# Optimization experiments

Measured on AMD Instinct MI355X. Metric: run time of the kernel, lower is better.

Reference implementation:

```python
import jax, jax.numpy as jnp
import numpy as np

TEMP = 0.1
TEMP_SUP = 0.5
PROP = 0.5  # proportion_pure_contrastive
SIGMA = 1.0
GAMMA = 1.0 / (2.0 * SIGMA ** 2)
INF = 1e8


def _l2norm(x, eps=1e-12):
    # torch F.normalize: x / max(||x||, eps)
    n = jnp.sqrt(jnp.sum(x * x, axis=-1, keepdims=True))
    return x / jnp.maximum(n, eps)


def _cross_entropy(logits, targets):
    # mean over rows of -log_softmax(logits)[i, targets[i]]
    logp = jax.nn.log_softmax(logits, axis=-1)
    return -jnp.mean(jnp.take_along_axis(logp, targets[:, None], axis=-1))


def setup_inputs() -> dict:
    key = jax.random.key(0)
    k1, k2, k3 = jax.random.split(key, 3)
    N, D = 4096, 256
    z_i = jax.random.normal(k1, (N, D), dtype=jnp.float32)
    z_j = jax.random.normal(k2, (N, D), dtype=jnp.float32)
    labels = jax.random.normal(k3, (N, 1), dtype=jnp.float32)
    return {"z_i": z_i, "z_j": z_j, "labels": labels}


def _forward(z_i, z_j, labels):
    N = z_i.shape[0]
    eye = jnp.eye(N, dtype=z_i.dtype)
    zin = _l2norm(z_i)
    zjn = _l2norm(z_j)

    # ---- pure contrastive branch (temperature TEMP) ----
    sim_zii = zin @ zin.T / TEMP - INF * eye
    sim_zjj = zjn @ zjn.T / TEMP - INF * eye
    sim_zij = zin @ zjn.T / TEMP
    correct = jnp.arange(N, dtype=jnp.int32)
    loss_i = _cross_entropy(jnp.concatenate([sim_zij, sim_zii], axis=1), correct)
    loss_j = _cross_entropy(jnp.concatenate([sim_zij.T, sim_zjj], axis=1), correct)
    loss_pure = loss_i + loss_j

    # ---- supervised branch (temperature TEMP_SUP) ----
    s_zii = zin @ zin.T / TEMP_SUP - INF * eye
    s_zjj = zjn @ zjn.T / TEMP_SUP - INF * eye
    s_zij = zin @ zjn.T / TEMP_SUP

    # RBF kernel on duplicated labels (detached in original -> stop_gradient)
    all_lab = jnp.tile(labels.reshape(N, -1), (2, 1))  # [2N, L]
    all_lab = jax.lax.stop_gradient(all_lab)
    sq = jnp.sum(all_lab * all_lab, axis=1)
    d2 = sq[:, None] + sq[None, :] - 2.0 * (all_lab @ all_lab.T)
    weights = jnp.exp(-GAMMA * jnp.maximum(d2, 0.0))  # [2N, 2N]
    weights = weights * (1.0 - jnp.eye(2 * N, dtype=weights.dtype))
    norm = jnp.sum(weights, axis=1, keepdims=True)  # [2N, 1]
    weights = weights / norm
    weights_norm = weights * jnp.log(norm)

    sim_Z = jnp.concatenate([
        jnp.concatenate([s_zii, s_zij], axis=1),
        jnp.concatenate([s_zij.T, s_zjj], axis=1),
    ], axis=0)  # [2N, 2N]
    log_sim_Z = jax.nn.log_softmax(sim_Z, axis=1)
    loss_sup = (-1.0 / N) * jnp.sum(weights * log_sim_Z)
    loss_sup += (-1.0 / N) * jnp.sum(weights_norm)

    return PROP * loss_pure + (1.0 - PROP) * loss_sup


def reference(z_i, z_j, labels):
    return _forward(z_i, z_j, labels)
```

## Files before the change

kernel.cpp:

```cpp
#include <hip/hip_runtime.h>
#include <hip/hip_bf16.h>

#define NN 4096
#define DD 256

typedef __attribute__((ext_vector_type(8))) short bf16x8;
typedef __attribute__((ext_vector_type(4))) float f32x4;

#define LOG2E 1.44269504088896f

typedef const unsigned int __attribute__((address_space(1)))* gu32p;
typedef unsigned int __attribute__((address_space(3)))* su32p;

__device__ __forceinline__ float fexp2(float x) { return __builtin_amdgcn_exp2f(x); }

__global__ __launch_bounds__(256) void k_norm(const float* __restrict__ zi,
                                              const float* __restrict__ zj,
                                              __hip_bfloat16* __restrict__ oi,
                                              __hip_bfloat16* __restrict__ oj) {
  int gw = (blockIdx.x * 256 + threadIdx.x) >> 6;
  int lane = threadIdx.x & 63;
  const float* src = (gw < NN) ? zi : zj;
  __hip_bfloat16* dst = (gw < NN) ? oi : oj;
  int row = (gw < NN) ? gw : gw - NN;
  float4 v = ((const float4*)(src + (size_t)row * DD))[lane];
  float ss = v.x * v.x + v.y * v.y + v.z * v.z + v.w * v.w;
#pragma unroll
  for (int m = 1; m < 64; m <<= 1) ss += __shfl_xor(ss, m);
  float s = 1.0f / fmaxf(sqrtf(ss), 1e-12f);
  __hip_bfloat16* d = dst + (size_t)row * DD + lane * 4;
  d[0] = __float2bfloat16(v.x * s);
  d[1] = __float2bfloat16(v.y * s);
  d[2] = __float2bfloat16(v.z * s);
  d[3] = __float2bfloat16(v.w * s);
}

template <int MODE>
__device__ __forceinline__ void epi(
    const f32x4 acc[2][4], const float labr[2][4], const float* __restrict__ labels,
    float rA[2][4], float rB[2][4], float rC[2][4], float rT[2][4],
    float* __restrict__ diag, int rowbase, int colbase, int wave, int fr, int kg) {
#pragma unroll
  for (int cf = 0; cf < 4; ++cf) {
    const int cg = colbase + cf * 16 + fr;
    const float labc = labels[cg];
#pragma unroll
    for (int sub = 0; sub < 2; ++sub) {
#pragma unroll
      for (int reg = 0; reg < 4; ++reg) {
        float S = acc[sub][cf][reg];
        float b = fexp2(fmaf(2.f * LOG2E, S, -2.f * LOG2E));
        float b2 = b * b;
        float b5 = b2 * b2 * b;
        float dl = labr[sub][reg] - labc;
        float kk = fexp2(dl * dl * (-0.5f * LOG2E));
        float ks = kk * S;
        if (MODE != 0) {
          const int rg = rowbase + wave * 32 + sub * 16 + kg * 4 + reg;
          if (MODE == 1) {
            if (rg == cg) diag[rg] = S;
          }
          if (MODE == 2) {
            if (rg == cg) { b = 0.f; b5 = 0.f; ks = 0.f; kk = 0.f; }
          }
        }
        rA[sub][reg] += b5;
        rB[sub][reg] += b;
        rC[sub][reg] += ks;
        rT[sub][reg] += kk;
      }
    }
  }
}

__global__ __launch_bounds__(256, 2) void k_main(
    const __hip_bfloat16* __restrict__ zin, const __hip_bfloat16* __restrict__ zjn,
    const float* __restrict__ labels,
    float* __restrict__ part, float* __restrict__ diag) {
  __shared__ short lB[64 * 256];

  const int cc = blockIdx.x;
  const int by = blockIdx.y;
  const int combo = blockIdx.z;

  const __hip_bfloat16* Ap = (combo == 1 || combo == 3) ? zjn : zin;
  const __hip_bfloat16* Bp = (combo == 1 || combo == 2) ? zin : zjn;
  const int rS0 = (combo == 0) ? 0 : (combo == 1) ? 2 : (combo == 2) ? 1 : 3;
  const bool wantT = (combo == 2);

  const int tid = threadIdx.x;
  const int lane = tid & 63;
  const int wave = tid >> 6;
  const int fr = lane & 15;
  const int kg = lane >> 4;
  const int rowbase = by * 128;
  char* lBc = (char*)lB;

  bf16x8 a[2][8];
#pragma unroll
  for (int sub = 0; sub < 2; ++sub) {
    const __hip_bfloat16* Ar =
        Ap + (size_t)(rowbase + wave * 32 + sub * 16 + fr) * DD + kg * 8;
#pragma unroll
    for (int k = 0; k < 8; ++k) a[sub][k] = *(const bf16x8*)(Ar + k * 32);
  }

  float labr[2][4];
#pragma unroll
  for (int sub = 0; sub < 2; ++sub)
#pragma unroll
    for (int reg = 0; reg < 4; ++reg)
      labr[sub][reg] = labels[rowbase + wave * 32 + sub * 16 + kg * 4 + reg];

  float rA[2][4] = {}, rB[2][4] = {}, rC[2][4] = {}, rT[2][4] = {};

  const int frb = (fr >> 2) & 1;
  const int P0 = fr * 512 + ((kg ^ (fr & 3)) << 4) + (frb << 6);

  const int dt0 = by * 2 - cc * 16;

#define STAGE(t)                                                              \
  {                                                                           \
    const char* Bt = (const char*)Bp + (size_t)(cc * 1024 + (t) * 64) * 512;  \
    _Pragma("unroll") for (int j = 0; j < 8; ++j) {                           \
      int f = tid + 256 * j;                                                  \
      int g = f ^ ((f >> 5) & 7);                                             \
      __builtin_amdgcn_global_load_lds(                                       \
          (gu32p)(const void*)(Bt + (size_t)g * 16),                          \
          (su32p)(void*)(lBc + (wave * 64 + 256 * j) * 16), 16, 0, 0);        \
    }                                                                         \
  }

  STAGE(0);

  for (int t = 0; t < 16; ++t) {
    __syncthreads();

    f32x4 acc[2][4];
#pragma unroll
    for (int s2 = 0; s2 < 2; ++s2)
#pragma unroll
      for (int cf = 0; cf < 4; ++cf) acc[s2][cf] = (f32x4){0.f, 0.f, 0.f, 0.f};

#pragma unroll
    for (int k = 0; k < 8; ++k) {
      const char* bbase = lBc + (P0 ^ (k << 6));
#pragma unroll
      for (int cf = 0; cf < 4; ++cf) {
        bf16x8 bv = *(const bf16x8*)(bbase + cf * 8192);
        acc[0][cf] = __builtin_amdgcn_mfma_f32_16x16x32_bf16(a[0][k], bv, acc[0][cf], 0, 0, 0);
        acc[1][cf] = __builtin_amdgcn_mfma_f32_16x16x32_bf16(a[1][k], bv, acc[1][cf], 0, 0, 0);
      }
    }

    __syncthreads();
    if (t < 15) STAGE(t + 1);

    const int colbase = cc * 1024 + t * 64;
    if (combo != 1 && (unsigned)(t - dt0) < 2u) {
      if (combo == 0)
        epi<1>(acc, labr, labels, rA, rB, rC, rT, diag, rowbase, colbase, wave, fr, kg);
      else
        epi<2>(acc, labr, labels, rA, rB, rC, rT, diag, rowbase, colbase, wave, fr, kg);
    } else {
      epi<0>(acc, labr, labels, rA, rB, rC, rT, diag, rowbase, colbase, wave, fr, kg);
    }
  }

  float* pc = part + (size_t)cc * 13 * NN;
#pragma unroll
  for (int sub = 0; sub < 2; ++sub)
#pragma unroll
    for (int reg = 0; reg < 4; ++reg) {
      float va = rA[sub][reg], vb = rB[sub][reg];
      float vc = rC[sub][reg], vt = rT[sub][reg];
#pragma unroll
      for (int m = 1; m < 16; m <<= 1) {
        va += __shfl_xor(va, m);
        vb += __shfl_xor(vb, m);
        vc += __shfl_xor(vc, m);
        vt += __shfl_xor(vt, m);
      }
      if (fr == 0) {
        int rg = rowbase + wave * 32 + sub * 16 + kg * 4 + reg;
        pc[rS0 * NN + rg] = va;
        pc[(rS0 + 4) * NN + rg] = vb;
        pc[(rS0 + 8) * NN + rg] = vc;
        if (wantT) pc[12 * NN + rg] = vt;
      }
    }
}

__global__ __launch_bounds__(256) void k_final(const float* __restrict__ part,
                                               const float* __restrict__ diag,
                                               float* __restrict__ out) {
  int i = blockIdx.x * 256 + threadIdx.x;
  float st[13];
#pragma unroll
  for (int p = 0; p < 13; ++p) {
    float s = 0.f;
#pragma unroll
    for (int c = 0; c < 4; ++c) s += part[((size_t)c * 13 + p) * NN + i];
    st[p] = s;
  }
  float d = diag[i];
  float accP = logf(st[0] + st[1]) + logf(st[2] + st[3]) + 20.f - 20.f * d;
  float nrm = 2.f * st[12] + 1.f;
  float W = 2.f * (st[8] + st[9] + st[10] + st[11]) / nrm;
  float lse = logf(st[4] + st[5]) + logf(st[6] + st[7]) + 4.f;
  float accS = lse - W - 2.f * logf(nrm);
  float v = accP + accS;
#pragma unroll
  for (int m = 1; m < 64; m <<= 1) v += __shfl_xor(v, m);
  __shared__ float red[4];
  if ((threadIdx.x & 63) == 0) red[threadIdx.x >> 6] = v;
  __syncthreads();
  if (threadIdx.x == 0) {
    float s = red[0] + red[1] + red[2] + red[3];
    atomicAdd(out, 0.5f * s / (float)NN);
  }
}

extern "C" void kernel_launch(void* const* d_in, const int* in_sizes, int n_in,
                              void* d_out, int out_size, void* d_ws, size_t ws_size,
                              hipStream_t stream) {
  const float* zi = (const float*)d_in[0];
  const float* zj = (const float*)d_in[1];
  const float* labels = (const float*)d_in[2];
  float* out = (float*)d_out;

  char* ws = (char*)d_ws;
  __hip_bfloat16* zinH = (__hip_bfloat16*)ws;
  __hip_bfloat16* zjnH = (__hip_bfloat16*)(ws + (size_t)NN * DD * 2);
  float* part = (float*)(ws + (size_t)NN * DD * 4);
  float* diag = part + 4 * 13 * NN;

  hipMemsetAsync(out, 0, sizeof(float), stream);

  k_norm<<<2 * NN / 4, 256, 0, stream>>>(zi, zj, zinH, zjnH);

  dim3 grid(4, NN / 128, 4);
  k_main<<<grid, 256, 0, stream>>>(zinH, zjnH, labels, part, diag);

  k_final<<<NN / 256, 256, 0, stream>>>(part, diag, out);
}
```

Before: 77.08 us.

## Exploit zi·zj transpose symmetry to drop fourth GEMM combo via column sums

Removes the separate zj·ziᵀ GEMM by computing column-wise partial sums (exp terms and kernel-weighted sims) of the zi·zjᵀ tile in the same pass, reducing work from four Gram blocks to three. It also splits columns across eight chunks instead of four, raises the occupancy hint to three blocks per CU, and packs the epilogue math into two-wide float vectors. The cost is extra shuffle reductions, shared-memory column buffers and a larger partial-sum buffer that the final kernel must read back. The label-kernel normalisation now comes from combo 0 rows, with the diagonal handled by a -1 correction.

```diff
diff --git a/kernel.cpp b/kernel.cpp
--- a/kernel.cpp
+++ b/kernel.cpp
@@ -3,11 +3,13 @@
 
 #define NN 4096
 #define DD 256
+#define CCN 8
+#define TPB 8
+#define LOG2E 1.44269504088896f
 
 typedef __attribute__((ext_vector_type(8))) short bf16x8;
 typedef __attribute__((ext_vector_type(4))) float f32x4;
-
-#define LOG2E 1.44269504088896f
+typedef __attribute__((ext_vector_type(2))) float f32x2;
 
 typedef const unsigned int __attribute__((address_space(1)))* gu32p;
 typedef unsigned int __attribute__((address_space(3)))* su32p;
@@ -35,58 +37,72 @@
   d[3] = __float2bfloat16(v.w * s);
 }
 
-template <int MODE>
+template <int MODE, bool COL>
 __device__ __forceinline__ void epi(
-    const f32x4 acc[2][4], const float labr[2][4], const float* __restrict__ labels,
-    float rA[2][4], float rB[2][4], float rC[2][4], float rT[2][4],
-    float* __restrict__ diag, int rowbase, int colbase, int wave, int fr, int kg) {
+    const f32x4 acc[2][4], const f32x2 labr[2][2], const float* __restrict__ labels,
+    f32x2 rA[2][2], f32x2 rB[2][2], f32x2 rC[2][2], f32x2 rT[2][2],
+    float cw[4][3], float* __restrict__ diag,
+    int rowbase, int colbase, int wave, int fr, int kg) {
 #pragma unroll
   for (int cf = 0; cf < 4; ++cf) {
     const int cg = colbase + cf * 16 + fr;
     const float labc = labels[cg];
+    const f32x2 labc2 = {labc, labc};
 #pragma unroll
     for (int sub = 0; sub < 2; ++sub) {
 #pragma unroll
-      for (int reg = 0; reg < 4; ++reg) {
-        float S = acc[sub][cf][reg];
-        float b = fexp2(fmaf(2.f * LOG2E, S, -2.f * LOG2E));
-        float b2 = b * b;
-        float b5 = b2 * b2 * b;
-        float dl = labr[sub][reg] - labc;
-        float kk = fexp2(dl * dl * (-0.5f * LOG2E));
-        float ks = kk * S;
+      for (int pp = 0; pp < 2; ++pp) {
+        f32x2 S = {acc[sub][cf][2 * pp], acc[sub][cf][2 * pp + 1]};
+        f32x2 arg = S * (2.f * LOG2E) + (-2.f * LOG2E);
+        f32x2 b;
+        b.x = fexp2(arg.x);
+        b.y = fexp2(arg.y);
+        f32x2 b2 = b * b;
+        f32x2 b5 = b2 * b2 * b;
+        f32x2 dl = labr[sub][pp] - labc2;
+        f32x2 e = (dl * (-0.5f * LOG2E)) * dl;
+        f32x2 kk;
+        kk.x = fexp2(e.x);
+        kk.y = fexp2(e.y);
+        f32x2 ks = kk * S;
         if (MODE != 0) {
-          const int rg = rowbase + wave * 32 + sub * 16 + kg * 4 + reg;
+          const int rg = rowbase + wave * 32 + sub * 16 + kg * 4 + 2 * pp;
           if (MODE == 1) {
-            if (rg == cg) diag[rg] = S;
+            if (rg == cg) diag[cg] = S.x;
+            if (rg + 1 == cg) diag[cg] = S.y;
+          } else {
+            if (rg == cg)     { b5.x = 0.f; b.x = 0.f; ks.x = 0.f; }
+            if (rg + 1 == cg) { b5.y = 0.f; b.y = 0.f; ks.y = 0.f; }
           }
-          if (MODE == 2) {
-            if (rg == cg) { b = 0.f; b5 = 0.f; ks = 0.f; kk = 0.f; }
-          }
-        }
-        rA[sub][reg] += b5;
-        rB[sub][reg] += b;
-        rC[sub][reg] += ks;
-        rT[sub][reg] += kk;
+        }
+        rA[sub][pp] += b5;
+        rB[sub][pp] += b;
+        rC[sub][pp] += ks;
+        if (COL) {
+          rT[sub][pp] += kk;
+          cw[cf][0] += b5.x + b5.y;
+          cw[cf][1] += b.x + b.y;
+          cw[cf][2] += ks.x + ks.y;
+        }
       }
     }
   }
 }
 
-__global__ __launch_bounds__(256, 2) void k_main(
+__global__ __launch_bounds__(256, 3) void k_main(
     const __hip_bfloat16* __restrict__ zin, const __hip_bfloat16* __restrict__ zjn,
     const float* __restrict__ labels,
-    float* __restrict__ part, float* __restrict__ diag) {
+    float* __restrict__ part, float* __restrict__ colp, float* __restrict__ diag) {
   __shared__ short lB[64 * 256];
+  __shared__ float colw[4][3][64];
 
   const int cc = blockIdx.x;
   const int by = blockIdx.y;
   const int combo = blockIdx.z;
-
-  const __hip_bfloat16* Ap = (combo == 1 || combo == 3) ? zjn : zin;
-  const __hip_bfloat16* Bp = (combo == 1 || combo == 2) ? zin : zjn;
-  const int rS0 = (combo == 0) ? 0 : (combo == 1) ? 2 : (combo == 2) ? 1 : 3;
-  const bool wantT = (combo == 2);
+  const bool COLF = (combo == 0);
+
+  const __hip_bfloat16* Ap = (combo == 2) ? zjn : zin;
+  const __hip_bfloat16* Bp = (combo == 1) ? zin : zjn;
 
   const int tid = threadIdx.x;
   const int lane = tid & 63;
@@ -105,36 +121,44 @@
     for (int k = 0; k < 8; ++k) a[sub][k] = *(const bf16x8*)(Ar + k * 32);
   }
 
-  float labr[2][4];
+  f32x2 labr[2][2];
 #pragma unroll
   for (int sub = 0; sub < 2; ++sub)
 #pragma unroll
-    for (int reg = 0; reg < 4; ++reg)
-      labr[sub][reg] = labels[rowbase + wave * 32 + sub * 16 + kg * 4 + reg];
-
-  float rA[2][4] = {}, rB[2][4] = {}, rC[2][4] = {}, rT[2][4] = {};
+    for (int pp = 0; pp < 2; ++pp) {
+      const float* lp = labels + rowbase + wave * 32 + sub * 16 + kg * 4 + 2 * pp;
+      labr[sub][pp] = (f32x2){lp[0], lp[1]};
+    }
+
+  f32x2 rA[2][2] = {}, rB[2][2] = {}, rC[2][2] = {}, rT[2][2] = {};
 
   const int frb = (fr >> 2) & 1;
   const int P0 = fr * 512 + ((kg ^ (fr & 3)) << 4) + (frb << 6);
 
-  const int dt0 = by * 2 - cc * 16;
-
-#define STAGE(t)                                                              \
-  {                                                                           \
-    const char* Bt = (const char*)Bp + (size_t)(cc * 1024 + (t) * 64) * 512;  \
-    _Pragma("unroll") for (int j = 0; j < 8; ++j) {                           \
-      int f = tid + 256 * j;                                                  \
-      int g = f ^ ((f >> 5) & 7);                                             \
-      __builtin_amdgcn_global_load_lds(                                       \
-          (gu32p)(const void*)(Bt + (size_t)g * 16),                          \
-          (su32p)(void*)(lBc + (wave * 64 + 256 * j) * 16), 16, 0, 0);        \
-    }                                                                         \
-  }
-
-  STAGE(0);
-
-  for (int t = 0; t < 16; ++t) {
+  auto stage = [&](int t) {
+    const char* Bt = (const char*)Bp + (size_t)(cc * 512 + t * 64) * 512;
+#pragma unroll
+    for (int j = 0; j < 8; ++j) {
+      int f = tid + 256 * j;
+      int g = f ^ ((f >> 5) & 7);
+      __builtin_amdgcn_global_load_lds(
+          (gu32p)(const void*)(Bt + (size_t)g * 16),
+          (su32p)(void*)(lBc + (wave * 64 + 256 * j) * 16), 16, 0, 0);
+    }
+  };
+  auto flushcol = [&](int t) {
+    if (tid < 192) {
+      int p = tid >> 6, c = tid & 63;
+      float v = colw[0][p][c] + colw[1][p][c] + colw[2][p][c] + colw[3][p][c];
+      colp[((size_t)(by * 64 + cc * TPB + t)) * 192 + p * 64 + c] = v;
+    }
+  };
+
+  stage(0);
+
+  for (int t = 0; t < TPB; ++t) {
     __syncthreads();
+    if (COLF && t > 0) flushcol(t - 1);
 
     f32x4 acc[2][4];
 #pragma unroll
@@ -154,71 +178,96 @@
     }
 
     __syncthreads();
-    if (t < 15) STAGE(t + 1);
-
-    const int colbase = cc * 1024 + t * 64;
-    if (combo != 1 && (unsigned)(t - dt0) < 2u) {
-      if (combo == 0)
-        epi<1>(acc, labr, labels, rA, rB, rC, rT, diag, rowbase, colbase, wave, fr, kg);
+    if (t < TPB - 1) stage(t + 1);
+
+    const int colbase = cc * 512 + t * 64;
+    const unsigned dtt = (unsigned)(cc * TPB + t - 2 * by);
+    float cw[4][3] = {};
+    if (COLF) {
+      if (dtt < 2u)
+        epi<1, true>(acc, labr, labels, rA, rB, rC, rT, cw, diag, rowbase, colbase, wave, fr, kg);
       else
-        epi<2>(acc, labr, labels, rA, rB, rC, rT, diag, rowbase, colbase, wave, fr, kg);
+        epi<0, true>(acc, labr, labels, rA, rB, rC, rT, cw, diag, rowbase, colbase, wave, fr, kg);
+#pragma unroll
+      for (int cf = 0; cf < 4; ++cf)
+#pragma unroll
+        for (int p = 0; p < 3; ++p) {
+          float v = cw[cf][p];
+          v += __shfl_xor(v, 16);
+          v += __shfl_xor(v, 32);
+          if (kg == 0) colw[wave][p][cf * 16 + fr] = v;
+        }
     } else {
-      epi<0>(acc, labr, labels, rA, rB, rC, rT, diag, rowbase, colbase, wave, fr, kg);
-    }
-  }
-
-  float* pc = part + (size_t)cc * 13 * NN;
+      if (dtt < 2u)
+        epi<2, false>(acc, labr, labels, rA, rB, rC, rT, cw, diag, rowbase, colbase, wave, fr, kg);
+      else
+        epi<0, false>(acc, labr, labels, rA, rB, rC, rT, cw, diag, rowbase, colbase, wave, fr, kg);
+    }
+  }
+
+  __syncthreads();
+  if (COLF) flushcol(TPB - 1);
+
+  float* pc = part + (size_t)cc * 10 * NN;
+  const int pr = combo;
 #pragma unroll
   for (int sub = 0; sub < 2; ++sub)
 #pragma unroll
-    for (int reg = 0; reg < 4; ++reg) {
-      float va = rA[sub][reg], vb = rB[sub][reg];
-      float vc = rC[sub][reg], vt = rT[sub][reg];
-#pragma unroll
-      for (int m = 1; m < 16; m <<= 1) {
-        va += __shfl_xor(va, m);
-        vb += __shfl_xor(vb, m);
-        vc += __shfl_xor(vc, m);
-        vt += __shfl_xor(vt, m);
+    for (int pp = 0; pp < 2; ++pp)
+#pragma unroll
+      for (int comp = 0; comp < 2; ++comp) {
+        float va = rA[sub][pp][comp], vb = rB[sub][pp][comp];
+        float vc = rC[sub][pp][comp], vt = rT[sub][pp][comp];
+#pragma unroll
+        for (int m = 1; m < 16; m <<= 1) {
+          va += __shfl_xor(va, m);
+          vb += __shfl_xor(vb, m);
+          vc += __shfl_xor(vc, m);
+          vt += __shfl_xor(vt, m);
+        }
+        if (fr == 0) {
+          int r = rowbase + wave * 32 + sub * 16 + kg * 4 + 2 * pp + comp;
+          pc[pr * NN + r] = va;
+          pc[(3 + pr) * NN + r] = vb;
+          pc[(6 + pr) * NN + r] = vc;
+          if (COLF) pc[9 * NN + r] = vt;
+        }
       }
-      if (fr == 0) {
-        int rg = rowbase + wave * 32 + sub * 16 + kg * 4 + reg;
-        pc[rS0 * NN + rg] = va;
-        pc[(rS0 + 4) * NN + rg] = vb;
-        pc[(rS0 + 8) * NN + rg] = vc;
-        if (wantT) pc[12 * NN + rg] = vt;
-      }
-    }
-}
-
-__global__ __launch_bounds__(256) void k_final(const float* __restrict__ part,
-                                               const float* __restrict__ diag,
-                                               float* __restrict__ out) {
-  int i = blockIdx.x * 256 + threadIdx.x;
-  float st[13];
-#pragma unroll
-  for (int p = 0; p < 13; ++p) {
+}
+
+__global__ __launch_bounds__(256) void k_final(
+    const float* __restrict__ part, const float* __restrict__ colp,
+    const float* __restrict__ diag, float* __restrict__ out) {
+  int r = blockIdx.x * 256 + threadIdx.x;
+  float st[10];
+#pragma unroll
+  for (int p = 0; p < 10; ++p) {
     float s = 0.f;
 #pragma unroll
-    for (int c = 0; c < 4; ++c) s += part[((size_t)c * 13 + p) * NN + i];
+    for (int c = 0; c < CCN; ++c) s += part[((size_t)c * 10 + p) * NN + r];
     st[p] = s;
   }
-  float d = diag[i];
-  float accP = logf(st[0] + st[1]) + logf(st[2] + st[3]) + 20.f - 20.f * d;
-  float nrm = 2.f * st[12] + 1.f;
-  float W = 2.f * (st[8] + st[9] + st[10] + st[11]) / nrm;
-  float lse = logf(st[4] + st[5]) + logf(st[6] + st[7]) + 4.f;
-  float accS = lse - W - 2.f * logf(nrm);
+  float a3 = 0.f, b3 = 0.f, c3 = 0.f;
+  const int ct = r >> 6, c63 = r & 63;
+  for (int by = 0; by < 32; ++by) {
+    const float* cp = colp + ((size_t)(by * 64 + ct)) * 192;
+    a3 += cp[c63];
+    b3 += cp[64 + c63];
+    c3 += cp[128 + c63];
+  }
+  float d = diag[r];
+  float accP = logf(st[0] + st[1]) + logf(a3 + st[2]) + 20.f - 20.f * d;
+  float nrm = 2.f * st[9] - 1.f;
+  float W = 2.f * (st[6] + st[7] + c3 + st[8]) / nrm;
+  float accS = logf(st[3] + st[4]) + logf(b3 + st[5]) + 4.f - W - 2.f * logf(nrm);
   float v = accP + accS;
 #pragma unroll
   for (int m = 1; m < 64; m <<= 1) v += __shfl_xor(v, m);
   __shared__ float red[4];
   if ((threadIdx.x & 63) == 0) red[threadIdx.x >> 6] = v;
   __syncthreads();
-  if (threadIdx.x == 0) {
-    float s = red[0] + red[1] + red[2] + red[3];
-    atomicAdd(out, 0.5f * s / (float)NN);
-  }
+  if (threadIdx.x == 0)
+    atomicAdd(out, 0.5f * (red[0] + red[1] + red[2] + red[3]) / (float)NN);
 }
 
 extern "C" void kernel_launch(void* const* d_in, const int* in_sizes, int n_in,
@@ -233,14 +282,15 @@
   __hip_bfloat16* zinH = (__hip_bfloat16*)ws;
   __hip_bfloat16* zjnH = (__hip_bfloat16*)(ws + (size_t)NN * DD * 2);
   float* part = (float*)(ws + (size_t)NN * DD * 4);
-  float* diag = part + 4 * 13 * NN;
+  float* colp = part + (size_t)CCN * 10 * NN;
+  float* diag = colp + (size_t)2048 * 192;
 
   hipMemsetAsync(out, 0, sizeof(float), stream);
 
   k_norm<<<2 * NN / 4, 256, 0, stream>>>(zi, zj, zinH, zjnH);
 
-  dim3 grid(4, NN / 128, 4);
-  k_main<<<grid, 256, 0, stream>>>(zinH, zjnH, labels, part, diag);
-
-  k_final<<<NN / 256, 256, 0, stream>>>(part, diag, out);
-}
+  dim3 grid(CCN, NN / 128, 3);
+  k_main<<<grid, 256, 0, stream>>>(zinH, zjnH, labels, part, colp, diag);
+
+  k_final<<<NN / 256, 256, 0, stream>>>(part, colp, diag, out);
+}
```

Measured after the change: 139.3 us. 1.81x slower.
